# Performance work log

Measured on AMD Instinct MI355X. Metric: run time of the kernel, lower is better.

The kernel has to match this reference:

```python
import jax, jax.numpy as jnp
import numpy as np

MRG = 0.1
ALPHA = 32.0
STAT_WEIGHT = 0.01
STAT_ADJUST_WEIGHT = 0.15
COS_EPS = 1e-8  # torch F.cosine_similarity eps


def l2_norm(x):
    # matches torch l2_norm: x / sqrt(sum(x^2, axis=1) + 1e-12)
    normp = jnp.sum(x * x, axis=1) + 1e-12
    return x / jnp.sqrt(normp)[:, None]


def setup_inputs() -> dict:
    key = jax.random.key(0)
    kx, kt, kp, kc = jax.random.split(key, 4)
    B, C, D = 512, 50000, 128
    X = jax.random.normal(kx, (B, D), dtype=jnp.float32)
    T = jax.random.randint(kt, (B,), 0, C, dtype=jnp.int32)
    proxies = jax.random.normal(kp, (C, D), dtype=jnp.float32)
    class_centers = jax.random.normal(kc, (C, D), dtype=jnp.float32)
    return {"X": X, "T": T, "proxies": proxies, "class_centers": class_centers}


def reference(X, T, proxies, class_centers):
    C = proxies.shape[0]
    Xn = l2_norm(X)                      # (B, D)
    Pn = l2_norm(proxies)                # (C, D)
    cos = Xn @ Pn.T                      # (B, C)

    # ---- vectorized per-class statistics (replaces the Python loop) ----
    counts = jax.ops.segment_sum(jnp.ones(T.shape[0], jnp.float32), T, num_segments=C)
    sums = jax.ops.segment_sum(Xn, T, num_segments=C)          # (C, D)
    sqs = jax.ops.segment_sum(Xn * Xn, T, num_segments=C)      # (C, D)
    safe = jnp.maximum(counts, 1.0)[:, None]
    mean = sums / safe
    var = jnp.clip(sqs / safe - mean * mean, 1e-6, 10.0)        # biased var, clamped
    var_weight = 1.0 / (1.0 + var.mean(axis=1))                 # (C,)

    # cosine_similarity(P_norm[i], class_centers[i]) with torch eps semantics
    pnorm = jnp.maximum(jnp.sqrt(jnp.sum(Pn * Pn, axis=1)), COS_EPS)
    cnorm = jnp.maximum(jnp.sqrt(jnp.sum(class_centers * class_centers, axis=1)), COS_EPS)
    center_sim = jnp.sum(Pn * class_centers, axis=1) / (pnorm * cnorm)  # (C,)

    has_samples = counts > 0
    adj = jnp.where(has_samples, center_sim * var_weight * STAT_ADJUST_WEIGHT, 0.0)
    combined = cos + adj[None, :]        # (B, C)

    # ---- proxy-anchor exp-sum terms ----
    onehot = (T[:, None] == jnp.arange(C, dtype=T.dtype)[None, :])  # (B, C) bool
    pos_exp = jnp.exp(-ALPHA * (combined - MRG))
    neg_exp = jnp.exp(ALPHA * (combined + MRG))
    P_sim_sum = jnp.sum(jnp.where(onehot, pos_exp, 0.0), axis=0)    # (C,)
    N_sim_sum = jnp.sum(jnp.where(onehot, 0.0, neg_exp), axis=0)    # (C,)

    num_valid = jnp.sum(has_samples).astype(jnp.float32)
    pos_term = jnp.sum(jnp.log1p(P_sim_sum)) / num_valid
    neg_term = jnp.sum(jnp.log1p(N_sim_sum)) / jnp.float32(C)

    center_reg = jnp.mean(jnp.abs(class_centers))
    return pos_term + neg_term + STAT_WEIGHT * center_reg
```

## Files before the change

### kernel.cpp

```cpp
#include <hip/hip_runtime.h>
#include <math.h>

#define ALPHA 32.0f
#define MRG 0.1f
#define STAT_WEIGHT 0.01f
#define STAT_ADJ_W 0.15f
#define COS_EPS 1e-8f

typedef __attribute__((ext_vector_type(8))) short bf16x8;
typedef __attribute__((ext_vector_type(4))) float f32x4;
typedef __attribute__((ext_vector_type(4))) unsigned int u32x4;

__device__ __forceinline__ ushort f2bf(float f) {
    unsigned u = __float_as_uint(f);
    return (ushort)((u + 0x7FFFu + ((u >> 16) & 1u)) >> 16);
}
__device__ __forceinline__ unsigned pk2(float a, float b) {
    return (unsigned)f2bf(a) | ((unsigned)f2bf(b) << 16);
}

__device__ __forceinline__ float bredL(float v, float* sm, int tid) {
    #pragma unroll
    for (int off = 1; off < 64; off <<= 1) v += __shfl_xor(v, off);
    if ((tid & 63) == 0 && tid < 128) sm[tid >> 6] = v;
    __syncthreads();
    float r = sm[0] + sm[1];
    __syncthreads();
    return r;
}

__global__ void k_stats(const float* __restrict__ X, const float* __restrict__ proxies,
                        const float* __restrict__ cc, const int* __restrict__ T,
                        ushort* __restrict__ Xn16, float* __restrict__ adj,
                        float* __restrict__ scal, float* __restrict__ cabs_part,
                        int C, int B) {
    const int tid = threadIdx.x, b = blockIdx.x;
    const int lane = tid & 63, wv = tid >> 6;
    const int d = tid & 127;
    const bool lo = tid < 128;
    __shared__ int Tl[512];
    __shared__ int mlist[512];
    __shared__ float sm[2];
    __shared__ float smc[4];
    __shared__ int mcnt;

    if (b == 0 && tid < 8) scal[tid] = 0.f;

    Tl[tid] = T[tid]; Tl[tid + 256] = T[tid + 256];
    if (tid == 0) mcnt = 0;

    float cabs = 0.f;
    {
        const float4* cp = (const float4*)cc;
        const int n4 = C * 32;
        #pragma unroll 4
        for (int i = b * 256 + tid; i < n4; i += B * 256) {
            float4 v = cp[i];
            cabs += fabsf(v.x) + fabsf(v.y) + fabsf(v.z) + fabsf(v.w);
        }
    }
    #pragma unroll
    for (int off = 1; off < 64; off <<= 1) cabs += __shfl_xor(cabs, off);
    if (lane == 0) smc[wv] = cabs;
    __syncthreads();
    if (tid == 0) cabs_part[b] = (smc[0] + smc[1]) + (smc[2] + smc[3]);

    const int c = Tl[b];

    {
        float x = lo ? X[(size_t)b * 128 + d] : 0.f;
        float n2 = bredL(x * x, sm, tid);
        float xn = x * rsqrtf(n2 + 1e-12f);
        if (lo) {
            const int pk = ((((d >> 3) ^ (b & 15)) << 3) | (d & 7));
            Xn16[(size_t)b * 128 + pk] = f2bf(xn);
        }
    }

    for (int j = tid; j < B; j += 256)
        if (Tl[j] == c) mlist[atomicAdd(&mcnt, 1)] = j;
    __syncthreads();
    const int cnt = mcnt;
    int minj = mlist[0];
    for (int i = 1; i < cnt; ++i) minj = min(minj, mlist[i]);
    if (minj != b) return;

    float sd = 0.f, qd = 0.f;
    int prev = -1;
    for (int rank = 0; rank < cnt; ++rank) {
        int cur = 0x7fffffff;
        for (int i = 0; i < cnt; ++i) { int v = mlist[i]; if (v > prev && v < cur) cur = v; }
        prev = cur;
        float xj = lo ? X[(size_t)cur * 128 + d] : 0.f;
        float nj = bredL(xj * xj, sm, tid);
        float xnj = xj * rsqrtf(nj + 1e-12f);
        sd += xnj; qd += xnj * xnj;
    }
    float fc = (float)cnt;
    float m = sd / fc;
    float var = fminf(fmaxf(qd / fc - m * m, 1e-6f), 10.0f);
    float sv = bredL(var, sm, tid);

    float p  = lo ? proxies[(size_t)c * 128 + d] : 0.f;
    float cv = lo ? cc[(size_t)c * 128 + d] : 0.f;
    float s2 = bredL(p * p, sm, tid);
    float c2 = bredL(cv * cv, sm, tid);
    float pc = bredL(p * cv, sm, tid);
    if (tid == 0) {
        float inv = rsqrtf(s2 + 1e-12f);
        float pn = fmaxf(sqrtf(s2) * inv, COS_EPS);
        float cn = fmaxf(sqrtf(c2), COS_EPS);
        float censim = (pc * inv) / (pn * cn);
        float vw = 1.0f / (1.0f + sv * (1.0f / 128.0f));
        adj[c] = censim * vw * STAT_ADJ_W;
    }
}

__launch_bounds__(256, 2)
__global__ void k_main(const float* __restrict__ proxies, const ushort* __restrict__ Xsw,
                       const int* __restrict__ T, float* __restrict__ PN,
                       int C, int nslice) {
    const int tid = threadIdx.x, lane = tid & 63, wv = tid >> 6;
    const int nlo = lane & 15, quad = lane >> 4;
    const int half = blockIdx.y;

    __shared__ ushort Sx[32768];
    __shared__ alignas(16) int Tl[256];

    {
        const uint4* src = (const uint4*)Xsw + half * 4096;
        uint4* dst = (uint4*)Sx;
        #pragma unroll
        for (int k = 0; k < 16; ++k) dst[tid + k * 256] = src[tid + k * 256];
    }
    Tl[tid] = T[half * 256 + tid];
    __syncthreads();

    float* PA = PN + (size_t)half * 2 * C;
    float* NA = PA + C;

    int fro[4];
    #pragma unroll
    for (int ks = 0; ks < 4; ++ks)
        fro[ks] = nlo * 128 + (((ks * 4 + quad) ^ nlo) << 3);

    const int s0 = (blockIdx.x + (half ? 128 : 0)) & 255;
    for (int s = s0; s < nslice; s += 256) {
        const int c0 = s * 128;
        const int cls0 = c0 + wv * 32 + nlo;
        const int cls1 = cls0 + 16;

        bf16x8 bfr[2][4];
        #pragma unroll
        for (int t = 0; t < 2; ++t) {
            int cls = c0 + wv * 32 + t * 16 + nlo;
            int cl = (cls < C) ? cls : C - 1;
            const float4* pr = (const float4*)(proxies + (size_t)cl * 128);
            float4 v0[4], v1[4];
            float s2 = 0.f;
            #pragma unroll
            for (int ks = 0; ks < 4; ++ks) {
                v0[ks] = pr[ks * 8 + quad * 2];
                v1[ks] = pr[ks * 8 + quad * 2 + 1];
                s2 += v0[ks].x*v0[ks].x + v0[ks].y*v0[ks].y + v0[ks].z*v0[ks].z + v0[ks].w*v0[ks].w
                    + v1[ks].x*v1[ks].x + v1[ks].y*v1[ks].y + v1[ks].z*v1[ks].z + v1[ks].w*v1[ks].w;
            }
            s2 += __shfl_xor(s2, 16);
            s2 += __shfl_xor(s2, 32);
            float pin = rsqrtf(s2 + 1e-12f);
            #pragma unroll
            for (int ks = 0; ks < 4; ++ks) {
                u32x4 u;
                u.x = pk2(v0[ks].x * pin, v0[ks].y * pin);
                u.y = pk2(v0[ks].z * pin, v0[ks].w * pin);
                u.z = pk2(v1[ks].x * pin, v1[ks].y * pin);
                u.w = pk2(v1[ks].z * pin, v1[ks].w * pin);
                bfr[t][ks] = __builtin_bit_cast(bf16x8, u);
            }
        }

        float pp0 = 0.f, np0 = 0.f, pp1 = 0.f, np1 = 0.f;
        #pragma unroll 4
        for (int rt = 0; rt < 16; ++rt) {
            const ushort* sb = &Sx[rt * 2048];
            bf16x8 a0 = *(const bf16x8*)&sb[fro[0]];
            bf16x8 a1 = *(const bf16x8*)&sb[fro[1]];
            bf16x8 a2 = *(const bf16x8*)&sb[fro[2]];
            bf16x8 a3 = *(const bf16x8*)&sb[fro[3]];
            f32x4 acc0 = {0.f,0.f,0.f,0.f}, acc1 = {0.f,0.f,0.f,0.f};
            acc0 = __builtin_amdgcn_mfma_f32_16x16x32_bf16(a0, bfr[0][0], acc0, 0, 0, 0);
            acc1 = __builtin_amdgcn_mfma_f32_16x16x32_bf16(a0, bfr[1][0], acc1, 0, 0, 0);
            acc0 = __builtin_amdgcn_mfma_f32_16x16x32_bf16(a1, bfr[0][1], acc0, 0, 0, 0);
            acc1 = __builtin_amdgcn_mfma_f32_16x16x32_bf16(a1, bfr[1][1], acc1, 0, 0, 0);
            acc0 = __builtin_amdgcn_mfma_f32_16x16x32_bf16(a2, bfr[0][2], acc0, 0, 0, 0);
            acc1 = __builtin_amdgcn_mfma_f32_16x16x32_bf16(a2, bfr[1][2], acc1, 0, 0, 0);
            acc0 = __builtin_amdgcn_mfma_f32_16x16x32_bf16(a3, bfr[0][3], acc0, 0, 0, 0);
            acc1 = __builtin_amdgcn_mfma_f32_16x16x32_bf16(a3, bfr[1][3], acc1, 0, 0, 0);

            int4 t4 = *(const int4*)&Tl[rt * 16 + quad * 4];
            int tvs[4] = {t4.x, t4.y, t4.z, t4.w};
            #pragma unroll
            for (int r = 0; r < 4; ++r) {
                { bool po = (tvs[r] == cls0); float v = acc0[r];
                  float e = __expf(po ? -ALPHA * (v - MRG) : ALPHA * (v + MRG));
                  pp0 += po ? e : 0.f; np0 += po ? 0.f : e; }
                { bool po = (tvs[r] == cls1); float v = acc1[r];
                  float e = __expf(po ? -ALPHA * (v - MRG) : ALPHA * (v + MRG));
                  pp1 += po ? e : 0.f; np1 += po ? 0.f : e; }
            }
        }

        pp0 += __shfl_xor(pp0, 16); pp0 += __shfl_xor(pp0, 32);
        np0 += __shfl_xor(np0, 16); np0 += __shfl_xor(np0, 32);
        pp1 += __shfl_xor(pp1, 16); pp1 += __shfl_xor(pp1, 32);
        np1 += __shfl_xor(np1, 16); np1 += __shfl_xor(np1, 32);
        if (quad == 0) {
            if (cls0 < C) { PA[cls0] = pp0; NA[cls0] = np0; }
            if (cls1 < C) { PA[cls1] = pp1; NA[cls1] = np1; }
        }
    }
}

__launch_bounds__(256)
__global__ void k_fin(const float* __restrict__ PN, const float* __restrict__ adj,
                      const float* __restrict__ cabs_part, float* __restrict__ scal,
                      float* __restrict__ out, int C, int nfin) {
    const int tid = threadIdx.x, lane = tid & 63, wv = tid >> 6;
    const int c = blockIdx.x * 256 + tid;
    __shared__ float red[4][3];
    float lp = 0.f, ln = 0.f, nv = 0.f;
    if (c < C) {
        float p = PN[c] + PN[2 * (size_t)C + c];
        float n = PN[(size_t)C + c] + PN[3 * (size_t)C + c];
        float a = 0.f;
        if (p > 0.f) { a = adj[c]; nv = 1.f; }
        lp = log1pf(p * __expf(-ALPHA * a));
        ln = log1pf(n * __expf( ALPHA * a));
    }
    #pragma unroll
    for (int off = 1; off < 64; off <<= 1) {
        lp += __shfl_xor(lp, off);
        ln += __shfl_xor(ln, off);
        nv += __shfl_xor(nv, off);
    }
    if (lane == 0) { red[wv][0] = lp; red[wv][1] = ln; red[wv][2] = nv; }
    __syncthreads();
    if (tid == 0) {
        atomicAdd(&scal[0], red[0][0] + red[1][0] + red[2][0] + red[3][0]);
        atomicAdd(&scal[1], red[0][1] + red[1][1] + red[2][1] + red[3][1]);
        atomicAdd(&scal[3], red[0][2] + red[1][2] + red[2][2] + red[3][2]);
    }
    if (blockIdx.x == 0) {
        float cb = cabs_part[tid] + cabs_part[tid + 256];
        #pragma unroll
        for (int off = 1; off < 64; off <<= 1) cb += __shfl_xor(cb, off);
        __syncthreads();
        if (lane == 0) red[wv][0] = cb;
        __syncthreads();
        if (tid == 0) atomicAdd(&scal[2], red[0][0] + red[1][0] + red[2][0] + red[3][0]);
    }
    if (tid == 0) {
        __threadfence();
        unsigned old = atomicAdd((unsigned*)(scal + 4), 1u);
        if (old == (unsigned)(nfin - 1)) {
            float S0 = atomicAdd(&scal[0], 0.f);
            float S1 = atomicAdd(&scal[1], 0.f);
            float S2 = atomicAdd(&scal[2], 0.f);
            float S3 = atomicAdd(&scal[3], 0.f);
            out[0] = S0 / S3 + S1 / (float)C + STAT_WEIGHT * (S2 / ((float)C * 128.f));
        }
    }
}

extern "C" void kernel_launch(void* const* d_in, const int* in_sizes, int n_in,
                              void* d_out, int out_size, void* d_ws, size_t ws_size,
                              hipStream_t stream) {
    const float* X       = (const float*)d_in[0];
    const int*   T       = (const int*)d_in[1];
    const float* proxies = (const float*)d_in[2];
    const float* cc      = (const float*)d_in[3];
    float* out = (float*)d_out;

    const int B = in_sizes[1];
    const int D = in_sizes[0] / B;
    const int C = in_sizes[2] / D;

    float*  PN   = (float*)d_ws;
    float*  scal = PN + 4 * (size_t)C;
    float*  cabs_part = scal + 8;
    float*  adj  = cabs_part + 512;
    ushort* Xn16 = (ushort*)(adj + C);

    const int nslice = (C + 127) / 128;
    const int nfin   = (C + 255) / 256;

    k_stats<<<B, 256, 0, stream>>>(X, proxies, cc, T, Xn16, adj, scal,
                                   cabs_part, C, B);
    k_main<<<dim3(256, 2), 256, 0, stream>>>(proxies, Xn16, T, PN, C, nslice);
    k_fin<<<nfin, 256, 0, stream>>>(PN, adj, cabs_part, scal, out, C, nfin);
}
```

Measured before the change: 128.6 us.

## Fuse stats kernel into main GEMM kernel and normalize X in-block

Merges the per-class statistics kernel into the main MFMA/exp-sum kernel, so a single launch of 512 blocks does both. Each block now L2-normalizes its half of X itself and packs it as bf16 straight into shared memory, which removes the Xn16 global round-trip and the dependency between the two kernels. After the main loop, the same block reuses its shared memory to run the stats, abs-sum and adj computation for one sample. This removes one launch and the serial gap between kernels. The cost is redundant X normalization in every block and the stats tail adding time to the blocks that own a class.

New measurement: 136.6 us. 6.3% more time.

```diff
diff --git a/kernel.cpp b/kernel.cpp
--- a/kernel.cpp
+++ b/kernel.cpp
@@ -29,111 +29,52 @@
     return r;
 }
 
-__global__ void k_stats(const float* __restrict__ X, const float* __restrict__ proxies,
-                        const float* __restrict__ cc, const int* __restrict__ T,
-                        ushort* __restrict__ Xn16, float* __restrict__ adj,
-                        float* __restrict__ scal, float* __restrict__ cabs_part,
-                        int C, int B) {
-    const int tid = threadIdx.x, b = blockIdx.x;
-    const int lane = tid & 63, wv = tid >> 6;
-    const int d = tid & 127;
-    const bool lo = tid < 128;
-    __shared__ int Tl[512];
-    __shared__ int mlist[512];
+__launch_bounds__(256, 2)
+__global__ void k_ms(const float* __restrict__ X, const float* __restrict__ proxies,
+                     const float* __restrict__ cc, const int* __restrict__ T,
+                     float* __restrict__ PN, float* __restrict__ adj,
+                     float* __restrict__ cabs_part, float* __restrict__ scal,
+                     int C, int B, int nslice) {
+    const int tid = threadIdx.x, lane = tid & 63, wv = tid >> 6;
+    const int nlo = lane & 15, quad = lane >> 4;
+    const int bid = blockIdx.x;
+    const int x = bid & 255, half = bid >> 8;
+
+    __shared__ ushort Sx[32768];
+    __shared__ alignas(16) int Tg[256];
     __shared__ float sm[2];
     __shared__ float smc[4];
     __shared__ int mcnt;
 
-    if (b == 0 && tid < 8) scal[tid] = 0.f;
-
-    Tl[tid] = T[tid]; Tl[tid + 256] = T[tid + 256];
-    if (tid == 0) mcnt = 0;
-
-    float cabs = 0.f;
+    if (bid == 0 && tid < 8) scal[tid] = 0.f;
+
     {
-        const float4* cp = (const float4*)cc;
-        const int n4 = C * 32;
-        #pragma unroll 4
-        for (int i = b * 256 + tid; i < n4; i += B * 256) {
-            float4 v = cp[i];
-            cabs += fabsf(v.x) + fabsf(v.y) + fabsf(v.z) + fabsf(v.w);
-        }
-    }
-    #pragma unroll
-    for (int off = 1; off < 64; off <<= 1) cabs += __shfl_xor(cabs, off);
-    if (lane == 0) smc[wv] = cabs;
-    __syncthreads();
-    if (tid == 0) cabs_part[b] = (smc[0] + smc[1]) + (smc[2] + smc[3]);
-
-    const int c = Tl[b];
-
-    {
-        float x = lo ? X[(size_t)b * 128 + d] : 0.f;
-        float n2 = bredL(x * x, sm, tid);
-        float xn = x * rsqrtf(n2 + 1e-12f);
-        if (lo) {
-            const int pk = ((((d >> 3) ^ (b & 15)) << 3) | (d & 7));
-            Xn16[(size_t)b * 128 + pk] = f2bf(xn);
-        }
-    }
-
-    for (int j = tid; j < B; j += 256)
-        if (Tl[j] == c) mlist[atomicAdd(&mcnt, 1)] = j;
-    __syncthreads();
-    const int cnt = mcnt;
-    int minj = mlist[0];
-    for (int i = 1; i < cnt; ++i) minj = min(minj, mlist[i]);
-    if (minj != b) return;
-
-    float sd = 0.f, qd = 0.f;
-    int prev = -1;
-    for (int rank = 0; rank < cnt; ++rank) {
-        int cur = 0x7fffffff;
-        for (int i = 0; i < cnt; ++i) { int v = mlist[i]; if (v > prev && v < cur) cur = v; }
-        prev = cur;
-        float xj = lo ? X[(size_t)cur * 128 + d] : 0.f;
-        float nj = bredL(xj * xj, sm, tid);
-        float xnj = xj * rsqrtf(nj + 1e-12f);
-        sd += xnj; qd += xnj * xnj;
-    }
-    float fc = (float)cnt;
-    float m = sd / fc;
-    float var = fminf(fmaxf(qd / fc - m * m, 1e-6f), 10.0f);
-    float sv = bredL(var, sm, tid);
-
-    float p  = lo ? proxies[(size_t)c * 128 + d] : 0.f;
-    float cv = lo ? cc[(size_t)c * 128 + d] : 0.f;
-    float s2 = bredL(p * p, sm, tid);
-    float c2 = bredL(cv * cv, sm, tid);
-    float pc = bredL(p * cv, sm, tid);
-    if (tid == 0) {
-        float inv = rsqrtf(s2 + 1e-12f);
-        float pn = fmaxf(sqrtf(s2) * inv, COS_EPS);
-        float cn = fmaxf(sqrtf(c2), COS_EPS);
-        float censim = (pc * inv) / (pn * cn);
-        float vw = 1.0f / (1.0f + sv * (1.0f / 128.0f));
-        adj[c] = censim * vw * STAT_ADJ_W;
-    }
-}
-
-__launch_bounds__(256, 2)
-__global__ void k_main(const float* __restrict__ proxies, const ushort* __restrict__ Xsw,
-                       const int* __restrict__ T, float* __restrict__ PN,
-                       int C, int nslice) {
-    const int tid = threadIdx.x, lane = tid & 63, wv = tid >> 6;
-    const int nlo = lane & 15, quad = lane >> 4;
-    const int half = blockIdx.y;
-
-    __shared__ ushort Sx[32768];
-    __shared__ alignas(16) int Tl[256];
-
-    {
-        const uint4* src = (const uint4*)Xsw + half * 4096;
-        uint4* dst = (uint4*)Sx;
-        #pragma unroll
-        for (int k = 0; k < 16; ++k) dst[tid + k * 256] = src[tid + k * 256];
-    }
-    Tl[tid] = T[half * 256 + tid];
+        const int row = tid;
+        const float4* xr = (const float4*)(X + (size_t)(half * 256 + row) * 128);
+        float s32[32];
+        #pragma unroll
+        for (int g = 0; g < 32; ++g) {
+            float4 v = xr[g];
+            s32[g] = (v.x * v.x + v.y * v.y) + (v.z * v.z + v.w * v.w);
+        }
+        #pragma unroll
+        for (int w = 16; w >= 1; w >>= 1)
+            #pragma unroll
+            for (int g = 0; g < w; ++g) s32[g] = s32[2 * g] + s32[2 * g + 1];
+        float pin = rsqrtf(s32[0] + 1e-12f);
+        uint4* dst = (uint4*)Sx + row * 16;
+        #pragma unroll
+        for (int g = 0; g < 16; ++g) {
+            float4 a = xr[g * 2], b4 = xr[g * 2 + 1];
+            u32x4 u;
+            u.x = pk2(a.x * pin, a.y * pin);
+            u.y = pk2(a.z * pin, a.w * pin);
+            u.z = pk2(b4.x * pin, b4.y * pin);
+            u.w = pk2(b4.z * pin, b4.w * pin);
+            dst[g ^ (row & 15)] = __builtin_bit_cast(uint4, u);
+        }
+    }
+    Tg[tid] = T[half * 256 + tid];
     __syncthreads();
 
     float* PA = PN + (size_t)half * 2 * C;
@@ -144,7 +85,7 @@
     for (int ks = 0; ks < 4; ++ks)
         fro[ks] = nlo * 128 + (((ks * 4 + quad) ^ nlo) << 3);
 
-    const int s0 = (blockIdx.x + (half ? 128 : 0)) & 255;
+    const int s0 = (x + (half ? 128 : 0)) & 255;
     for (int s = s0; s < nslice; s += 256) {
         const int c0 = s * 128;
         const int cls0 = c0 + wv * 32 + nlo;
@@ -197,7 +138,7 @@
             acc0 = __builtin_amdgcn_mfma_f32_16x16x32_bf16(a3, bfr[0][3], acc0, 0, 0, 0);
             acc1 = __builtin_amdgcn_mfma_f32_16x16x32_bf16(a3, bfr[1][3], acc1, 0, 0, 0);
 
-            int4 t4 = *(const int4*)&Tl[rt * 16 + quad * 4];
+            int4 t4 = *(const int4*)&Tg[rt * 16 + quad * 4];
             int tvs[4] = {t4.x, t4.y, t4.z, t4.w};
             #pragma unroll
             for (int r = 0; r < 4; ++r) {
@@ -218,6 +159,72 @@
             if (cls0 < C) { PA[cls0] = pp0; NA[cls0] = np0; }
             if (cls1 < C) { PA[cls1] = pp1; NA[cls1] = np1; }
         }
+    }
+
+    __syncthreads();
+    int* Tl = (int*)Sx;
+    int* mlist = (int*)Sx + 512;
+    const int b = bid;
+    const int d = tid & 127;
+    const bool lo = tid < 128;
+
+    Tl[tid] = T[tid]; Tl[tid + 256] = T[tid + 256];
+    if (tid == 0) mcnt = 0;
+
+    float cabs = 0.f;
+    {
+        const float4* cp = (const float4*)cc;
+        const int n4 = C * 32;
+        #pragma unroll 4
+        for (int i = b * 256 + tid; i < n4; i += B * 256) {
+            float4 v = cp[i];
+            cabs += fabsf(v.x) + fabsf(v.y) + fabsf(v.z) + fabsf(v.w);
+        }
+    }
+    #pragma unroll
+    for (int off = 1; off < 64; off <<= 1) cabs += __shfl_xor(cabs, off);
+    if (lane == 0) smc[wv] = cabs;
+    __syncthreads();
+    if (tid == 0) cabs_part[b] = (smc[0] + smc[1]) + (smc[2] + smc[3]);
+
+    const int c = Tl[b];
+
+    for (int j = tid; j < B; j += 256)
+        if (Tl[j] == c) mlist[atomicAdd(&mcnt, 1)] = j;
+    __syncthreads();
+    const int cnt = mcnt;
+    int minj = mlist[0];
+    for (int i = 1; i < cnt; ++i) minj = min(minj, mlist[i]);
+    if (minj != b) return;
+
+    float sd = 0.f, qd = 0.f;
+    int prev = -1;
+    for (int rank = 0; rank < cnt; ++rank) {
+        int cur = 0x7fffffff;
+        for (int i = 0; i < cnt; ++i) { int v = mlist[i]; if (v > prev && v < cur) cur = v; }
+        prev = cur;
+        float xj = lo ? X[(size_t)cur * 128 + d] : 0.f;
+        float nj = bredL(xj * xj, sm, tid);
+        float xnj = xj * rsqrtf(nj + 1e-12f);
+        sd += xnj; qd += xnj * xnj;
+    }
+    float fc = (float)cnt;
+    float m = sd / fc;
+    float var = fminf(fmaxf(qd / fc - m * m, 1e-6f), 10.0f);
+    float sv = bredL(var, sm, tid);
+
+    float p  = lo ? proxies[(size_t)c * 128 + d] : 0.f;
+    float cv = lo ? cc[(size_t)c * 128 + d] : 0.f;
+    float s2 = bredL(p * p, sm, tid);
+    float c2 = bredL(cv * cv, sm, tid);
+    float pc = bredL(p * cv, sm, tid);
+    if (tid == 0) {
+        float inv = rsqrtf(s2 + 1e-12f);
+        float pn = fmaxf(sqrtf(s2) * inv, COS_EPS);
+        float cn = fmaxf(sqrtf(c2), COS_EPS);
+        float censim = (pc * inv) / (pn * cn);
+        float vw = 1.0f / (1.0f + sv * (1.0f / 128.0f));
+        adj[c] = censim * vw * STAT_ADJ_W;
     }
 }
 
@@ -289,13 +296,11 @@
     float*  scal = PN + 4 * (size_t)C;
     float*  cabs_part = scal + 8;
     float*  adj  = cabs_part + 512;
-    ushort* Xn16 = (ushort*)(adj + C);
 
     const int nslice = (C + 127) / 128;
     const int nfin   = (C + 255) / 256;
 
-    k_stats<<<B, 256, 0, stream>>>(X, proxies, cc, T, Xn16, adj, scal,
-                                   cabs_part, C, B);
-    k_main<<<dim3(256, 2), 256, 0, stream>>>(proxies, Xn16, T, PN, C, nslice);
+    k_ms<<<B, 256, 0, stream>>>(X, proxies, cc, T, PN, adj, cabs_part,
+                                scal, C, B, nslice);
     k_fin<<<nfin, 256, 0, stream>>>(PN, adj, cabs_part, scal, out, C, nfin);
 }
```
